# Optimization experiments

Measured on AMD Instinct MI355X. Metric: run time of the kernel, lower is better.

Reference implementation:

```python
import jax, jax.numpy as jnp
import numpy as np
import math

STRIDE = 32
CTR_CLAMP = 32.0
SCALE_CLAMP = math.log(1000.0 / 16)  # DEFAULT_SCALE_CLAMP
CONF_THRESH = 0.05
NMS_THRESH = 0.6
TOPK = 1000
NUM_CLASSES = 80
CLASS_OFFSET = 1.0e5  # separates classes so one IoU pass == per-class NMS


def setup_inputs() -> dict:
    key = jax.random.key(0)
    k1, k2 = jax.random.split(key)
    fmp_h, fmp_w = 100, 100
    A = 5
    M = fmp_h * fmp_w * A  # 50000 candidates
    cls_pred = jax.random.normal(k1, (M, NUM_CLASSES), dtype=jnp.float32)
    reg_pred = jax.random.normal(k2, (M, 4), dtype=jnp.float32)
    anchor_size = jnp.array([[32, 32], [64, 64], [128, 128], [256, 256], [512, 512]], dtype=jnp.float32)
    return {"cls_pred": cls_pred, "reg_pred": reg_pred, "anchor_size": anchor_size,
            "fmp_h": fmp_h, "fmp_w": fmp_w}


def _generate_anchors(anchor_size, fmp_h, fmp_w):
    # anchors laid out as [H*W, A, 4] -> [M, 4], matching torch.meshgrid order
    ys, xs = jnp.meshgrid(jnp.arange(fmp_h, dtype=jnp.float32),
                          jnp.arange(fmp_w, dtype=jnp.float32), indexing="ij")
    xy = (jnp.stack([xs, ys], axis=-1).reshape(-1, 2) + 0.5) * STRIDE  # [HW, 2]
    A = anchor_size.shape[0]
    anchor_xy = jnp.repeat(xy[:, None, :], A, axis=1)                   # [HW, A, 2]
    anchor_wh = jnp.broadcast_to(anchor_size[None], (xy.shape[0], A, 2))
    return jnp.concatenate([anchor_xy, anchor_wh], axis=-1).reshape(-1, 4)  # [M, 4]


def _decode_boxes(anchors, reg):
    # anchors/reg: [K, 4] (cx, cy, w, h) / (dx, dy, dw, dh)
    ctr_off = jnp.clip(reg[:, :2] * anchors[:, 2:], -CTR_CLAMP, CTR_CLAMP)
    ctr_xy = anchors[:, :2] + ctr_off
    wh = anchors[:, 2:] * jnp.exp(jnp.minimum(reg[:, 2:], SCALE_CLAMP))
    return jnp.concatenate([ctr_xy - 0.5 * wh, ctr_xy + 0.5 * wh], axis=-1)  # x1y1x2y2


def _greedy_nms_keep(boxes, valid):
    # boxes: [K, 4] already score-sorted descending; valid: [K] bool
    x1, y1, x2, y2 = boxes[:, 0], boxes[:, 1], boxes[:, 2], boxes[:, 3]
    areas = (x2 - x1) * (y2 - y1)
    xx1 = jnp.maximum(x1[:, None], x1[None, :])
    yy1 = jnp.maximum(y1[:, None], y1[None, :])
    xx2 = jnp.minimum(x2[:, None], x2[None, :])
    yy2 = jnp.minimum(y2[:, None], y2[None, :])
    inter = jnp.maximum(1e-28, xx2 - xx1) * jnp.maximum(1e-28, yy2 - yy1)
    iou = inter / (areas[:, None] + areas[None, :] - inter + 1e-14)  # [K, K]
    idxs = jnp.arange(boxes.shape[0])

    def body(i, keep):
        suppress = keep[i] & (iou[i] > NMS_THRESH) & (idxs > i)
        return keep & ~suppress

    return jax.lax.fori_loop(0, boxes.shape[0], body, valid)


def reference(cls_pred, reg_pred, anchor_size, fmp_h, fmp_w):
    anchors = _generate_anchors(anchor_size, fmp_h, fmp_w)  # [M, 4]
    probs = jax.nn.sigmoid(cls_pred)                        # [M, C]
    scores = probs.max(axis=-1)
    labels = probs.argmax(axis=-1)
    # top-k candidates (lax.top_k returns scores sorted descending)
    scores, idx = jax.lax.top_k(scores, TOPK)
    labels = labels[idx]
    reg = reg_pred[idx]
    anc = anchors[idx]
    boxes = _decode_boxes(anc, reg)                         # [K, 4] in pixels
    valid = scores >= CONF_THRESH
    # per-class NMS via class offsets (boxes of different classes never overlap)
    boxes_off = boxes + labels.astype(boxes.dtype)[:, None] * CLASS_OFFSET
    keep = _greedy_nms_keep(boxes_off, valid)
    img_w = fmp_w * STRIDE
    img_h = fmp_h * STRIDE
    scale = jnp.array([img_w, img_h, img_w, img_h], dtype=boxes.dtype)
    nboxes = jnp.clip(boxes / scale, 0.0, 1.0)
    m = keep.astype(boxes.dtype)
    return nboxes * m[:, None], scores * m, jnp.where(keep, labels, -1), keep
```

## Files before the change

kernel.cpp:

```cpp
#include <hip/hip_runtime.h>
#include <math.h>

#define NCLS 80
#define TOPK 1000
#define CAND_CAP 4096
#define TRI_IDX(f, g) ((f) * 16 - ((f) * ((f) - 1)) / 2 + ((g) - (f)))

__device__ __forceinline__ float sigmoid_np(float x) {
  float e = (float)exp(-(double)x);
  return 1.0f / (1.0f + e);
}
__device__ __forceinline__ float exp_np(float x) { return (float)exp((double)x); }

__device__ __forceinline__ unsigned fkey(float s) {
  unsigned u = __float_as_uint(s);
  return ((int)u < 0) ? ~u : (u | 0x80000000u);
}

#define KEY_BASE 0xBF000000u
__device__ __forceinline__ unsigned kbin(unsigned key) { return (key >> 11) & 0xFFFu; }

__device__ __forceinline__ void agg_add(unsigned* h, unsigned bin, bool pred) {
  unsigned long long rem = __ballot(pred);
  const int lane = threadIdx.x & 63;
  while (rem) {
    int leader = __ffsll(rem) - 1;
    unsigned lb = (unsigned)__shfl((int)bin, leader, 64);
    unsigned long long m = __ballot(pred && bin == lb);
    if (lane == leader) atomicAdd(&h[lb], (unsigned)__popcll(m));
    rem &= ~m;
  }
}

__global__ void k_zero(unsigned* __restrict__ p, int nwords) {
  int i = blockIdx.x * 256 + threadIdx.x;
  if (i < nwords) p[i] = 0u;
}

__launch_bounds__(1024)
__global__ void k_score(const float* __restrict__ cls, float* __restrict__ scores,
                        int* __restrict__ labels, unsigned* __restrict__ ghist1, int M) {
  __shared__ unsigned h1[4096];
  const int t = threadIdx.x;
  #pragma unroll
  for (int k = 0; k < 4; ++k) h1[t + 1024 * k] = 0u;
  __syncthreads();

  int gid = blockIdx.x * 1024 + t;
  int anchor = gid >> 2;
  int q = gid & 3;
  bool act = anchor < M;
  float lv[20];
  float best = -3.4e38f; int bc = 0;
  if (act) {
    const float4* row = reinterpret_cast<const float4*>(cls) + (size_t)anchor * (NCLS / 4);
    #pragma unroll
    for (int k = 0; k < 5; ++k) {
      float4 v = row[q + 4 * k];
      int cbase = (q + 4 * k) * 4;
      lv[4 * k + 0] = v.x; lv[4 * k + 1] = v.y; lv[4 * k + 2] = v.z; lv[4 * k + 3] = v.w;
      if (v.x > best) { best = v.x; bc = cbase + 0; }
      if (v.y > best) { best = v.y; bc = cbase + 1; }
      if (v.z > best) { best = v.z; bc = cbase + 2; }
      if (v.w > best) { best = v.w; bc = cbase + 3; }
    }
  } else {
    #pragma unroll
    for (int k = 0; k < 20; ++k) lv[k] = -3.4e38f;
  }
  #pragma unroll
  for (int d = 1; d < 4; d <<= 1) {
    float ob = __shfl_xor(best, d, 64);
    int oc = __shfl_xor(bc, d, 64);
    if (ob > best || (ob == best && oc < bc)) { best = ob; bc = oc; }
  }
  float s = sigmoid_np(best);
  float sp = s * (1.0f - s);
  float band = (s < 1.0f && sp > 0.0f) ? (4.8e-7f / sp) : 3.4e38f;
  float thresh = best - band;
  int cclose = 1 << 30;
  #pragma unroll
  for (int k = 0; k < 5; ++k) {
    #pragma unroll
    for (int j = 0; j < 4; ++j) {
      int c = (q + 4 * k) * 4 + j;
      if (lv[4 * k + j] >= thresh && c < cclose) cclose = c;
    }
  }
  #pragma unroll
  for (int d = 1; d < 4; d <<= 1) {
    int oc = __shfl_xor(cclose, d, 64);
    if (oc < cclose) cclose = oc;
  }
  int lab = bc;
  if (act && cclose < bc && q == 0) {
    float bp = -1.0f; int bl = 0;
    for (int c = 0; c < NCLS; ++c) {
      float p = sigmoid_np(cls[(size_t)anchor * NCLS + c]);
      if (p > bp) { bp = p; bl = c; }
    }
    lab = bl;
  }
  unsigned key = fkey(s);
  if (act && q == 0) {
    scores[anchor] = s;
    labels[anchor] = lab;
  }
  agg_add(h1, kbin(key), act && q == 0 && key >= KEY_BASE);
  __syncthreads();
  #pragma unroll
  for (int k = 0; k < 4; ++k) {
    unsigned c = h1[t + 1024 * k];
    if (c) atomicAdd(&ghist1[t + 1024 * k], c);
  }
}

__launch_bounds__(1024)
__global__ void k_compact(const unsigned* __restrict__ ghist1, const float* __restrict__ scores,
                          unsigned long long* __restrict__ cand, unsigned* __restrict__ gcount,
                          int M) {
  __shared__ unsigned chunks[1024];
  __shared__ int sB1;
  __shared__ unsigned wcnt[16];
  __shared__ unsigned sbase;
  const int t = threadIdx.x;
  const int lane = t & 63, wid = t >> 6;
  if (t == 0) sB1 = 0;

  unsigned hb0 = ghist1[4 * t], hb1 = ghist1[4 * t + 1],
           hb2 = ghist1[4 * t + 2], hb3 = ghist1[4 * t + 3];
  chunks[t] = hb0 + hb1 + hb2 + hb3;
  __syncthreads();
  for (int d = 1; d < 1024; d <<= 1) {
    unsigned v = chunks[t] + ((t + d < 1024) ? chunks[t + d] : 0u);
    __syncthreads(); chunks[t] = v; __syncthreads();
  }
  {
    unsigned ssc = chunks[t];
    unsigned ssn = (t + 1 < 1024) ? chunks[t + 1] : 0u;
    if (ssc >= (unsigned)TOPK && ssn < (unsigned)TOPK) {
      unsigned hb[4] = {hb0, hb1, hb2, hb3};
      unsigned run = ssn;
      for (int b = 3; b >= 0; --b) {
        run += hb[b];
        if (run >= (unsigned)TOPK) { sB1 = 4 * t + b; break; }
      }
    }
  }
  __syncthreads();
  const unsigned T = KEY_BASE + ((unsigned)sB1 << 11);

  int base = (blockIdx.x * 1024 + t) * 4;
  unsigned keys[4]; int idxs[4]; int np = 0;
  if (base + 3 < M) {
    float4 v = *reinterpret_cast<const float4*>(scores + base);
    unsigned kk[4] = {fkey(v.x), fkey(v.y), fkey(v.z), fkey(v.w)};
    #pragma unroll
    for (int j = 0; j < 4; ++j)
      if (kk[j] >= T) { keys[np] = kk[j]; idxs[np] = base + j; ++np; }
  } else {
    for (int i = base; i < M; ++i) {
      unsigned key = fkey(scores[i]);
      if (key >= T) { keys[np] = key; idxs[np] = i; ++np; }
    }
  }
  int sc = np;
  #pragma unroll
  for (int d = 1; d < 64; d <<= 1) {
    int o = __shfl_up(sc, d, 64);
    if (lane >= d) sc += o;
  }
  if (lane == 63) wcnt[wid] = (unsigned)sc;
  __syncthreads();
  if (t == 0) {
    unsigned acc = 0;
    for (int w = 0; w < 16; ++w) { unsigned v = wcnt[w]; wcnt[w] = acc; acc += v; }
    sbase = acc ? atomicAdd(gcount, acc) : 0u;
  }
  __syncthreads();
  unsigned pos = sbase + wcnt[wid] + (unsigned)(sc - np);
  for (int j = 0; j < np; ++j) {
    if (pos < (unsigned)CAND_CAP)
      cand[pos] = ((unsigned long long)keys[j] << 32) | (unsigned)(~(unsigned)idxs[j]);
    ++pos;
  }
}

__launch_bounds__(1024)
__global__ void k_maskr(const unsigned long long* __restrict__ cand,
                        const unsigned* __restrict__ gcount,
                        const int* __restrict__ labels, const float* __restrict__ reg,
                        const float* __restrict__ asz, const int* __restrict__ pW, int A,
                        float* __restrict__ sel_score, int* __restrict__ sel_label,
                        float* __restrict__ boxes,
                        unsigned long long* __restrict__ maskC) {
  __shared__ unsigned long long ck[CAND_CAP];
  __shared__ float so0[1024], so1[1024], so2[1024], so3[1024], sa[1024];
  __shared__ float4 bx[1024];
  __shared__ float ssc[1024]; __shared__ int slab[1024];
  const int t = threadIdx.x;
  const int c = blockIdx.x;

  ssc[t] = 0.0f; slab[t] = 0;
  so0[t] = 0.0f; so1[t] = 0.0f; so2[t] = 0.0f; so3[t] = 0.0f; sa[t] = 0.0f;
  unsigned n = *gcount; if (n > (unsigned)CAND_CAP) n = (unsigned)CAND_CAP;
  for (int i = t; i < (int)n; i += 1024) ck[i] = cand[i];
  __syncthreads();

  for (int cc = 0; cc < CAND_CAP; cc += 1024) {
    if ((unsigned)cc >= n) break;
    int cidx = cc + t;
    if ((unsigned)cidx < n) {
      unsigned long long my = ck[cidx];
      int r = 0;
      for (int j = 0; j < (int)n; ++j) r += (ck[j] > my);
      if (r < TOPK) {
        unsigned key = (unsigned)(my >> 32);
        unsigned u = (key & 0x80000000u) ? (key ^ 0x80000000u) : ~key;
        float scv = __uint_as_float(u);
        int idx = (int)(~(unsigned)my);
        int lab = labels[idx];
        int W = *pW;
        int a = idx % A;
        int cell = idx / A;
        int x = cell % W;
        int y = cell / W;
        float aw = asz[a * 2 + 0], ah = asz[a * 2 + 1];
        float ax = ((float)x + 0.5f) * 32.0f;
        float ay = ((float)y + 0.5f) * 32.0f;
        float4 rg = *reinterpret_cast<const float4*>(reg + (size_t)idx * 4);
        float offx = fminf(fmaxf(rg.x * aw, -32.0f), 32.0f);
        float offy = fminf(fmaxf(rg.y * ah, -32.0f), 32.0f);
        float cx = ax + offx, cy = ay + offy;
        const float SC = 4.135166556742356f;
        float bw = aw * exp_np(fminf(rg.z, SC));
        float bh = ah * exp_np(fminf(rg.w, SC));
        float x1 = cx - 0.5f * bw, y1 = cy - 0.5f * bh;
        float x2 = cx + 0.5f * bw, y2 = cy + 0.5f * bh;
        float off = (float)lab * 100000.0f;
        float ox1 = x1 + off, oy1 = y1 + off, ox2 = x2 + off, oy2 = y2 + off;
        ssc[r] = scv; slab[r] = lab;
        bx[r] = make_float4(x1, y1, x2, y2);
        so0[r] = ox1; so1[r] = oy1; so2[r] = ox2; so3[r] = oy2;
        sa[r] = (ox2 - ox1) * (oy2 - oy1);
      }
    }
  }
  __syncthreads();

  if (c == 0) {
    sel_score[t] = ssc[t];
    sel_label[t] = slab[t];
    reinterpret_cast<float4*>(boxes)[t] = bx[t];
  }

  {
    int j = t;
    unsigned long long bits = 0ull;
    if (j < TOPK) {
      float x1j = so0[j], y1j = so1[j], x2j = so2[j], y2j = so3[j];
      float aj = sa[j];
      int i0 = c * 64;
      for (int ii = 0; ii < 64; ++ii) {
        int i = i0 + ii;
        if (i < TOPK && i < j) {
          float xx1 = fmaxf(so0[i], x1j);
          float yy1 = fmaxf(so1[i], y1j);
          float xx2 = fminf(so2[i], x2j);
          float yy2 = fminf(so3[i], y2j);
          float inter = fmaxf(1e-28f, xx2 - xx1) * fmaxf(1e-28f, yy2 - yy1);
          float uni = sa[i] + aj - inter + 1e-14f;
          float iou = inter / uni;
          if (iou > 0.6f) bits |= (1ull << ii);
        }
      }
    }
    maskC[c * 1024 + j] = bits;
  }
}

__launch_bounds__(1024)
__global__ void k_nms(const unsigned long long* __restrict__ maskC,
                      const float* __restrict__ sel_score, const int* __restrict__ sel_label,
                      const float* __restrict__ boxes,
                      const int* __restrict__ pW, const int* __restrict__ pH,
                      float* __restrict__ out) {
  __shared__ unsigned long long sm[136 * 64];
  __shared__ float ssc[1024];
  __shared__ unsigned long long kwS[16];
  __shared__ int pf[136], pg[136];
  const int t = threadIdx.x;
  const int lane = t & 63;

  if (t < 136) {
    int p = t, f = 0;
    while (p >= 16 - f) { p -= 16 - f; ++f; }
    pf[t] = f; pg[t] = f + p;
  }
  ssc[t] = (t < TOPK) ? sel_score[t] : 0.0f;
  __syncthreads();
  for (int i = t; i < 136 * 64; i += 1024) {
    int p = i >> 6, l = i & 63;
    sm[i] = maskC[pf[p] * 1024 + pg[p] * 64 + l];
  }
  __syncthreads();

  if (t < 64) {
    unsigned long long supp[16];
    #pragma unroll
    for (int f = 0; f < 16; ++f) supp[f] = 0ull;
    #pragma unroll
    for (int f = 0; f < 16; ++f) {
      unsigned long long ct = sm[TRI_IDX(f, f) * 64 + lane];
      int r = f * 64 + lane;
      unsigned long long valid = __ballot((r < TOPK) && (ssc[r] >= 0.05f));
      unsigned long long sup_any = __ballot(ct != 0ull);
      unsigned long long avail = valid & ~supp[f];
      unsigned long long kwf = 0ull;
      while (avail) {
        unsigned long long fs = avail & sup_any;
        if (!fs) { kwf |= avail; break; }
        int i = __ffsll((long long)fs) - 1;
        unsigned long long below = (1ull << i) - 1ull;
        kwf |= avail & below;
        kwf |= (1ull << i);
        unsigned long long vict = __ballot(((ct >> i) & 1ull) != 0ull);
        avail &= ~vict;
        avail &= ~(below | (1ull << i));
      }
      if (lane == 0) kwS[f] = kwf;
      #pragma unroll
      for (int g = f + 1; g < 16; ++g)
        supp[g] |= __ballot((sm[TRI_IDX(f, g) * 64 + lane] & kwf) != 0ull);
    }
  }
  __syncthreads();

  float sw = (float)(*pW * 32);
  float sh = (float)(*pH * 32);
  const float4* b4 = reinterpret_cast<const float4*>(boxes);
  if (t < TOPK) {
    int r = t;
    bool kp = (kwS[r >> 6] >> (r & 63)) & 1ull;
    float m = kp ? 1.0f : 0.0f;
    float4 b = b4[r];
    float b0 = fminf(fmaxf(b.x / sw, 0.0f), 1.0f) * m;
    float b1 = fminf(fmaxf(b.y / sh, 0.0f), 1.0f) * m;
    float b2 = fminf(fmaxf(b.z / sw, 0.0f), 1.0f) * m;
    float b3 = fminf(fmaxf(b.w / sh, 0.0f), 1.0f) * m;
    out[r * 4 + 0] = b0; out[r * 4 + 1] = b1;
    out[r * 4 + 2] = b2; out[r * 4 + 3] = b3;
    out[TOPK * 4 + r] = ssc[r] * m;
    out[TOPK * 5 + r] = kp ? (float)sel_label[r] : -1.0f;
    out[TOPK * 6 + r] = m;
  }
}

extern "C" void kernel_launch(void* const* d_in, const int* in_sizes, int n_in,
                              void* d_out, int out_size, void* d_ws, size_t ws_size,
                              hipStream_t stream) {
  const float* cls = (const float*)d_in[0];
  const float* reg = (const float*)d_in[1];
  const float* asz = (const float*)d_in[2];
  const int* pH = (const int*)d_in[3];
  const int* pW = (const int*)d_in[4];
  int M = in_sizes[0] / NCLS;
  int A = in_sizes[2] / 2;

  char* ws = (char*)d_ws;
  size_t off = 0;
  auto alloc = [&](size_t bytes) { size_t o = off; off = (off + bytes + 255) & ~(size_t)255; return o; };
  size_t o_h1   = alloc(4096 * sizeof(unsigned));
  size_t o_cnt  = alloc(256);
  size_t zero_end = off;
  size_t o_cand = alloc((size_t)CAND_CAP * sizeof(unsigned long long));
  size_t o_sc   = alloc((size_t)M * sizeof(float));
  size_t o_lb   = alloc((size_t)M * sizeof(int));
  size_t o_ssc  = alloc(1024 * sizeof(float));
  size_t o_slb  = alloc(1024 * sizeof(int));
  size_t o_box  = alloc(1024 * 4 * sizeof(float));
  size_t o_mask = alloc((size_t)16 * 1024 * sizeof(unsigned long long));
  (void)ws_size; (void)out_size; (void)n_in;

  int zwords = (int)(zero_end / 4);
  k_zero<<<(zwords + 255) / 256, 256, 0, stream>>>((unsigned*)ws, zwords);
  int nblk_score = (M * 4 + 1023) / 1024;
  k_score<<<nblk_score, 1024, 0, stream>>>(
      cls, (float*)(ws + o_sc), (int*)(ws + o_lb), (unsigned*)(ws + o_h1), M);
  int nblk_cmp = ((M + 3) / 4 + 1023) / 1024;
  k_compact<<<nblk_cmp, 1024, 0, stream>>>(
      (const unsigned*)(ws + o_h1), (const float*)(ws + o_sc),
      (unsigned long long*)(ws + o_cand), (unsigned*)(ws + o_cnt), M);
  k_maskr<<<16, 1024, 0, stream>>>(
      (const unsigned long long*)(ws + o_cand), (const unsigned*)(ws + o_cnt),
      (const int*)(ws + o_lb), reg, asz, pW, A,
      (float*)(ws + o_ssc), (int*)(ws + o_slb), (float*)(ws + o_box),
      (unsigned long long*)(ws + o_mask));
  k_nms<<<1, 1024, 0, stream>>>(
      (const unsigned long long*)(ws + o_mask),
      (const float*)(ws + o_ssc), (const int*)(ws + o_slb),
      (const float*)(ws + o_box), pW, pH, (float*)d_out);
}
```

Before: 72.65 us.

## Drop zero kernel and global histogram; rebuild histogram per block in compact

Removes the separate zeroing kernel and the global-atomic histogram built in the score kernel. Each compact block now rebuilds the full 4096-bin score histogram in shared memory by reading all scores, and the score kernel resets the candidate counter itself. This saves one kernel launch and the global atomics, at the cost of every compact block redundantly scanning all M scores and doing shared-memory atomics without warp aggregation.

```diff
diff --git a/kernel.cpp b/kernel.cpp
--- a/kernel.cpp
+++ b/kernel.cpp
@@ -18,33 +18,12 @@
 }
 
 #define KEY_BASE 0xBF000000u
-__device__ __forceinline__ unsigned kbin(unsigned key) { return (key >> 11) & 0xFFFu; }
-
-__device__ __forceinline__ void agg_add(unsigned* h, unsigned bin, bool pred) {
-  unsigned long long rem = __ballot(pred);
-  const int lane = threadIdx.x & 63;
-  while (rem) {
-    int leader = __ffsll(rem) - 1;
-    unsigned lb = (unsigned)__shfl((int)bin, leader, 64);
-    unsigned long long m = __ballot(pred && bin == lb);
-    if (lane == leader) atomicAdd(&h[lb], (unsigned)__popcll(m));
-    rem &= ~m;
-  }
-}
-
-__global__ void k_zero(unsigned* __restrict__ p, int nwords) {
-  int i = blockIdx.x * 256 + threadIdx.x;
-  if (i < nwords) p[i] = 0u;
-}
 
 __launch_bounds__(1024)
 __global__ void k_score(const float* __restrict__ cls, float* __restrict__ scores,
-                        int* __restrict__ labels, unsigned* __restrict__ ghist1, int M) {
-  __shared__ unsigned h1[4096];
+                        int* __restrict__ labels, unsigned* __restrict__ gcount, int M) {
   const int t = threadIdx.x;
-  #pragma unroll
-  for (int k = 0; k < 4; ++k) h1[t + 1024 * k] = 0u;
-  __syncthreads();
+  if (blockIdx.x == 0 && t == 0) *gcount = 0u;
 
   int gid = blockIdx.x * 1024 + t;
   int anchor = gid >> 2;
@@ -101,34 +80,46 @@
     }
     lab = bl;
   }
-  unsigned key = fkey(s);
   if (act && q == 0) {
     scores[anchor] = s;
     labels[anchor] = lab;
   }
-  agg_add(h1, kbin(key), act && q == 0 && key >= KEY_BASE);
-  __syncthreads();
-  #pragma unroll
-  for (int k = 0; k < 4; ++k) {
-    unsigned c = h1[t + 1024 * k];
-    if (c) atomicAdd(&ghist1[t + 1024 * k], c);
-  }
 }
 
 __launch_bounds__(1024)
-__global__ void k_compact(const unsigned* __restrict__ ghist1, const float* __restrict__ scores,
+__global__ void k_compact(const float* __restrict__ scores,
                           unsigned long long* __restrict__ cand, unsigned* __restrict__ gcount,
                           int M) {
+  __shared__ unsigned hist[4096];
   __shared__ unsigned chunks[1024];
   __shared__ int sB1;
   __shared__ unsigned wcnt[16];
   __shared__ unsigned sbase;
   const int t = threadIdx.x;
   const int lane = t & 63, wid = t >> 6;
+  const int M4 = M >> 2;
+  const float4* s4 = reinterpret_cast<const float4*>(scores);
   if (t == 0) sB1 = 0;
-
-  unsigned hb0 = ghist1[4 * t], hb1 = ghist1[4 * t + 1],
-           hb2 = ghist1[4 * t + 2], hb3 = ghist1[4 * t + 3];
+  #pragma unroll
+  for (int k = 0; k < 4; ++k) hist[t + 1024 * k] = 0u;
+  __syncthreads();
+
+  for (int i = t; i < M4; i += 1024) {
+    float4 v = s4[i];
+    unsigned k0 = fkey(v.x), k1 = fkey(v.y), k2 = fkey(v.z), k3 = fkey(v.w);
+    if (k0 >= KEY_BASE) atomicAdd(&hist[(k0 >> 11) & 0xFFFu], 1u);
+    if (k1 >= KEY_BASE) atomicAdd(&hist[(k1 >> 11) & 0xFFFu], 1u);
+    if (k2 >= KEY_BASE) atomicAdd(&hist[(k2 >> 11) & 0xFFFu], 1u);
+    if (k3 >= KEY_BASE) atomicAdd(&hist[(k3 >> 11) & 0xFFFu], 1u);
+  }
+  for (int i = M4 * 4 + t; i < M; i += 1024) {
+    unsigned k0 = fkey(scores[i]);
+    if (k0 >= KEY_BASE) atomicAdd(&hist[(k0 >> 11) & 0xFFFu], 1u);
+  }
+  __syncthreads();
+
+  unsigned hb0 = hist[4 * t], hb1 = hist[4 * t + 1],
+           hb2 = hist[4 * t + 2], hb3 = hist[4 * t + 3];
   chunks[t] = hb0 + hb1 + hb2 + hb3;
   __syncthreads();
   for (int d = 1; d < 1024; d <<= 1) {
@@ -370,9 +361,7 @@
   char* ws = (char*)d_ws;
   size_t off = 0;
   auto alloc = [&](size_t bytes) { size_t o = off; off = (off + bytes + 255) & ~(size_t)255; return o; };
-  size_t o_h1   = alloc(4096 * sizeof(unsigned));
   size_t o_cnt  = alloc(256);
-  size_t zero_end = off;
   size_t o_cand = alloc((size_t)CAND_CAP * sizeof(unsigned long long));
   size_t o_sc   = alloc((size_t)M * sizeof(float));
   size_t o_lb   = alloc((size_t)M * sizeof(int));
@@ -382,14 +371,12 @@
   size_t o_mask = alloc((size_t)16 * 1024 * sizeof(unsigned long long));
   (void)ws_size; (void)out_size; (void)n_in;
 
-  int zwords = (int)(zero_end / 4);
-  k_zero<<<(zwords + 255) / 256, 256, 0, stream>>>((unsigned*)ws, zwords);
   int nblk_score = (M * 4 + 1023) / 1024;
   k_score<<<nblk_score, 1024, 0, stream>>>(
-      cls, (float*)(ws + o_sc), (int*)(ws + o_lb), (unsigned*)(ws + o_h1), M);
+      cls, (float*)(ws + o_sc), (int*)(ws + o_lb), (unsigned*)(ws + o_cnt), M);
   int nblk_cmp = ((M + 3) / 4 + 1023) / 1024;
   k_compact<<<nblk_cmp, 1024, 0, stream>>>(
-      (const unsigned*)(ws + o_h1), (const float*)(ws + o_sc),
+      (const float*)(ws + o_sc),
       (unsigned long long*)(ws + o_cand), (unsigned*)(ws + o_cnt), M);
   k_maskr<<<16, 1024, 0, stream>>>(
       (const unsigned long long*)(ws + o_cand), (const unsigned*)(ws + o_cnt),
```

New measurement: 69.42 us. -4.5%, faster.
